# Kernel tuning notes

Measured on AMD Instinct MI355X. Metric: run time of the kernel, lower is better.

Reference implementation:

```python
import jax, jax.numpy as jnp
import numpy as np

N = 12000
E = 384000
F_IN, F_HID, F_OUT = 4, 50, 1433
NEG_SLOPE = 0.2  # PyG GATConv default leaky_relu slope


def gat_conv(x, W, a_src, a_dst, b, src, dst):
    """PyG GATConv (heads=1, concat=True) with self-loops already appended.
    x: [N, Fin], W: [Fin, Fout], a_src/a_dst/b: [Fout], src/dst: [E']."""
    h = x @ W                                   # [N, Fout]
    al = h @ a_src                              # [N] per-source logit part
    ar = h @ a_dst                              # [N] per-target logit part
    e = jax.nn.leaky_relu(al[src] + ar[dst], NEG_SLOPE)   # [E'] edge logits
    # segment softmax over edges grouped by destination node
    m = jax.ops.segment_max(e, dst, num_segments=N)       # [N]
    ex = jnp.exp(e - m[dst])
    s = jax.ops.segment_sum(ex, dst, num_segments=N)      # [N]
    alpha = ex / s[dst]                         # [E'] (self-loops => s > 0)
    out = jax.ops.segment_sum(alpha[:, None] * h[src], dst, num_segments=N)
    return out + b


def setup_inputs() -> dict:
    key = jax.random.key(0)
    ks = jax.random.split(key, 10)
    x = jax.random.normal(ks[0], (N, F_IN), dtype=jnp.float32)
    edge_index = jax.random.randint(ks[1], (2, E), 0, N, dtype=jnp.int32)
    # Glorot-ish init for params
    W1 = jax.random.normal(ks[2], (F_IN, F_HID), dtype=jnp.float32) / np.sqrt(F_IN)
    a_src1 = jax.random.normal(ks[3], (F_HID,), dtype=jnp.float32) / np.sqrt(F_HID)
    a_dst1 = jax.random.normal(ks[4], (F_HID,), dtype=jnp.float32) / np.sqrt(F_HID)
    b1 = jnp.zeros((F_HID,), dtype=jnp.float32)
    W2 = jax.random.normal(ks[5], (F_HID, F_OUT), dtype=jnp.float32) / np.sqrt(F_HID)
    a_src2 = jax.random.normal(ks[6], (F_OUT,), dtype=jnp.float32) / np.sqrt(F_OUT)
    a_dst2 = jax.random.normal(ks[7], (F_OUT,), dtype=jnp.float32) / np.sqrt(F_OUT)
    b2 = jnp.zeros((F_OUT,), dtype=jnp.float32)
    return {"x": x, "edge_index": edge_index, "W1": W1, "a_src1": a_src1,
            "a_dst1": a_dst1, "b1": b1, "W2": W2, "a_src2": a_src2,
            "a_dst2": a_dst2, "b2": b2}


def reference(x, edge_index, W1, a_src1, a_dst1, b1, W2, a_src2, a_dst2, b2):
    # PyG GATConv adds self-loops by default
    loops = jnp.arange(N, dtype=edge_index.dtype)
    src = jnp.concatenate([edge_index[0], loops])
    dst = jnp.concatenate([edge_index[1], loops])
    h = jax.nn.relu(gat_conv(x, W1, a_src1, a_dst1, b1, src, dst))
    h = jax.nn.relu(gat_conv(h, W2, a_src2, a_dst2, b2, src, dst))
    adj_pred = jax.nn.sigmoid(h @ h.T)          # InnerProductDecoder.forward_all
    return (adj_pred, edge_index)
```

## Files before the change

### kernel.cpp

```cpp
#include <hip/hip_runtime.h>
#include <hip/hip_bf16.h>

#define NNODES 12000
#define NEDGES 384000
#define NETOT  (NEDGES + NNODES)
#define FIN    4
#define FHID   50
#define FOUT   1433
#define KP     1440
#define MP     12032
#define NTILE  (MP / 128)
#define NTRI   (NTILE * (NTILE + 1) / 2)
#define NEG_SLOPE 0.2f

typedef __hip_bfloat16 bf16_t;
typedef __bf16 bf16x8 __attribute__((ext_vector_type(8)));
typedef float f32x4 __attribute__((ext_vector_type(4)));
typedef float f32x2 __attribute__((ext_vector_type(2)));

__device__ __forceinline__ float  b2f(bf16_t h) { return __bfloat162float(h); }
__device__ __forceinline__ bf16_t f2b(float f)  { return __float2bfloat16(f); }
__device__ __forceinline__ unsigned short f2bu(float f) { bf16_t h = f2b(f); return *(unsigned short*)&h; }

__global__ void k_init(int* __restrict__ deg, bf16_t* __restrict__ h2) {
    int i = blockIdx.x * blockDim.x + threadIdx.x;
    int stride = gridDim.x * blockDim.x;
    for (int v = i; v < NNODES; v += stride) deg[v] = 1;
    const size_t padN = (size_t)(MP - NNODES) * KP;
    for (size_t t = i; t < padN; t += stride) h2[(size_t)NNODES * KP + t] = f2b(0.f);
}

__global__ void k_count(const int* __restrict__ ei, int* __restrict__ deg) {
    int i = blockIdx.x * blockDim.x + threadIdx.x;
    if (i < NEDGES) atomicAdd(&deg[ei[NEDGES + i]], 1);
}

__global__ __launch_bounds__(1024) void k_scan(const int* __restrict__ deg, int* __restrict__ rowptr) {
    __shared__ int sd[1024];
    __shared__ int carry;
    int tid = threadIdx.x;
    if (tid == 0) { carry = 0; rowptr[0] = 0; }
    __syncthreads();
    for (int base = 0; base < NNODES; base += 1024) {
        int v = (base + tid < NNODES) ? deg[base + tid] : 0;
        sd[tid] = v;
        __syncthreads();
        for (int off = 1; off < 1024; off <<= 1) {
            int t = (tid >= off) ? sd[tid - off] : 0;
            __syncthreads();
            sd[tid] += t;
            __syncthreads();
        }
        int inc = sd[tid] + carry;
        if (base + tid < NNODES) rowptr[base + tid + 1] = inc;
        __syncthreads();
        if (tid == 1023) carry = sd[1023] + carry;
        __syncthreads();
    }
}

__global__ void k_cursor(const int* __restrict__ rowptr, int* __restrict__ cursor) {
    int i = blockIdx.x * blockDim.x + threadIdx.x;
    if (i < NNODES) cursor[i] = rowptr[i];
}

__global__ void k_fill(const int* __restrict__ ei, int* __restrict__ cursor, int* __restrict__ csrc) {
    int i = blockIdx.x * blockDim.x + threadIdx.x;
    if (i < NETOT) {
        int s, d;
        if (i < NEDGES) { s = ei[i]; d = ei[NEDGES + i]; }
        else            { s = d = i - NEDGES; }
        int pos = atomicAdd(&cursor[d], 1);
        csrc[pos] = s;
    }
}

__global__ __launch_bounds__(256) void k_linear1(
        const bf16_t* __restrict__ x, const bf16_t* __restrict__ W1,
        const bf16_t* __restrict__ as1, const bf16_t* __restrict__ ad1,
        float* __restrict__ h1pre, float* __restrict__ al, float* __restrict__ ar) {
    __shared__ float sW[FIN * FHID];
    __shared__ float sa[FHID], sdl[FHID];
    int tid = threadIdx.x;
    if (tid < FIN * FHID) sW[tid] = b2f(W1[tid]);
    if (tid < FHID) { sa[tid] = b2f(as1[tid]); sdl[tid] = b2f(ad1[tid]); }
    __syncthreads();
    int i = blockIdx.x * 256 + tid;
    if (i >= NNODES) return;
    float x0 = b2f(x[i * 4 + 0]), x1 = b2f(x[i * 4 + 1]);
    float x2 = b2f(x[i * 4 + 2]), x3 = b2f(x[i * 4 + 3]);
    float hal = 0.f, har = 0.f;
    for (int j = 0; j < FHID; ++j) {
        float h = x0 * sW[j] + x1 * sW[FHID + j] + x2 * sW[2 * FHID + j] + x3 * sW[3 * FHID + j];
        h1pre[(size_t)i * FHID + j] = h;
        hal += h * sa[j];
        har += h * sdl[j];
    }
    al[i] = hal; ar[i] = har;
}

__global__ __launch_bounds__(64) void k_agg1(
        const float* __restrict__ h1pre, const float* __restrict__ al, const float* __restrict__ ar,
        const int* __restrict__ rowptr, const int* __restrict__ csrc,
        const bf16_t* __restrict__ b1, float* __restrict__ h1) {
    int v = blockIdx.x, tid = threadIdx.x;
    int s0 = rowptr[v], s1 = rowptr[v + 1];
    float arv = ar[v];
    float m = -1e30f;
    for (int e = s0 + tid; e < s1; e += 64) {
        float l = al[csrc[e]] + arv;
        l = l > 0.f ? l : NEG_SLOPE * l;
        m = fmaxf(m, l);
    }
#pragma unroll
    for (int off = 32; off; off >>= 1) m = fmaxf(m, __shfl_xor(m, off, 64));
    __shared__ float sw[64];
    __shared__ int ssrc[64];
    float acc = 0.f, ssum = 0.f;
    for (int base = s0; base < s1; base += 64) {
        int e = base + tid;
        float w = 0.f; int si = 0;
        if (e < s1) {
            si = csrc[e];
            float l = al[si] + arv;
            l = l > 0.f ? l : NEG_SLOPE * l;
            w = __expf(l - m);
        }
        ssum += w;
        sw[tid] = w; ssrc[tid] = si;
        __syncthreads();
        int cnt = min(64, s1 - base);
        if (tid < FHID) {
#pragma unroll 4
            for (int j = 0; j < cnt; ++j)
                acc += sw[j] * h1pre[(size_t)ssrc[j] * FHID + tid];
        }
        __syncthreads();
    }
#pragma unroll
    for (int off = 32; off; off >>= 1) ssum += __shfl_xor(ssum, off, 64);
    if (tid < FHID) {
        float o = acc / ssum + b2f(b1[tid]);
        h1[(size_t)v * FHID + tid] = fmaxf(o, 0.f);
    }
}

__global__ __launch_bounds__(256) void k_linear2(
        const float* __restrict__ h1, const bf16_t* __restrict__ W2,
        const bf16_t* __restrict__ as2, const bf16_t* __restrict__ ad2,
        unsigned char* __restrict__ h2pre, float* __restrict__ al2, float* __restrict__ ar2) {
    int v0 = blockIdx.x * 4, tid = threadIdx.x;
    __shared__ float sh[4][FHID];
    if (tid < 4 * FHID) sh[tid / FHID][tid % FHID] = h1[(size_t)v0 * FHID + tid];
    __syncthreads();
    float pal[4] = {0.f, 0.f, 0.f, 0.f}, par[4] = {0.f, 0.f, 0.f, 0.f};
#pragma unroll
    for (int i = 0; i < 3; ++i) {
        int f0 = i * 512 + 2 * tid;
        if (f0 < KP) {
            float d0[4] = {0.f, 0.f, 0.f, 0.f}, d1[4] = {0.f, 0.f, 0.f, 0.f};
            bool ok0 = f0 < FOUT, ok1 = f0 + 1 < FOUT;
            if (ok0) {
                int f1 = ok1 ? f0 + 1 : f0;
#pragma unroll 10
                for (int k = 0; k < FHID; ++k) {
                    float w0 = b2f(W2[k * FOUT + f0]);
                    float w1 = b2f(W2[k * FOUT + f1]);
#pragma unroll
                    for (int c = 0; c < 4; ++c) {
                        d0[c] += sh[c][k] * w0;
                        d1[c] += sh[c][k] * w1;
                    }
                }
                if (!ok1) { d1[0] = d1[1] = d1[2] = d1[3] = 0.f; }
                float sa0 = b2f(as2[f0]), sd0 = b2f(ad2[f0]);
                float sa1 = ok1 ? b2f(as2[f0 + 1]) : 0.f;
                float sd1 = ok1 ? b2f(ad2[f0 + 1]) : 0.f;
#pragma unroll
                for (int c = 0; c < 4; ++c) {
                    pal[c] += d0[c] * sa0 + d1[c] * sa1;
                    par[c] += d0[c] * sd0 + d1[c] * sd1;
                }
            }
#pragma unroll
            for (int c = 0; c < 4; ++c) {
                int pk = __builtin_amdgcn_cvt_pk_fp8_f32(d0[c], d1[c], 0, false);
                *(unsigned short*)(h2pre + (size_t)(v0 + c) * KP + f0) = (unsigned short)pk;
            }
        }
    }
#pragma unroll
    for (int off = 32; off; off >>= 1)
#pragma unroll
        for (int c = 0; c < 4; ++c) {
            pal[c] += __shfl_xor(pal[c], off, 64);
            par[c] += __shfl_xor(par[c], off, 64);
        }
    __shared__ float rA[4][4], rB[4][4];
    int wave = tid >> 6, lane = tid & 63;
    if (lane == 0)
#pragma unroll
        for (int c = 0; c < 4; ++c) { rA[wave][c] = pal[c]; rB[wave][c] = par[c]; }
    __syncthreads();
    if (tid < 4) {
        al2[v0 + tid] = rA[0][tid] + rA[1][tid] + rA[2][tid] + rA[3][tid];
        ar2[v0 + tid] = rB[0][tid] + rB[1][tid] + rB[2][tid] + rB[3][tid];
    }
}

__global__ __launch_bounds__(256) void k_agg2(
        const unsigned char* __restrict__ h2pre, const float* __restrict__ al, const float* __restrict__ ar,
        const int* __restrict__ rowptr, const int* __restrict__ csrc,
        const bf16_t* __restrict__ bias2, bf16_t* __restrict__ h2) {
    int v = blockIdx.x, tid = threadIdx.x;
    int s0 = rowptr[v], s1 = rowptr[v + 1];
    float arv = ar[v];
    float m = -1e30f;
    for (int e = s0 + tid; e < s1; e += 256) {
        float l = al[csrc[e]] + arv;
        l = l > 0.f ? l : NEG_SLOPE * l;
        m = fmaxf(m, l);
    }
#pragma unroll
    for (int off = 32; off; off >>= 1) m = fmaxf(m, __shfl_xor(m, off, 64));
    __shared__ float red[4];
    int wave = tid >> 6, lane = tid & 63;
    if (lane == 0) red[wave] = m;
    __syncthreads();
    m = fmaxf(fmaxf(red[0], red[1]), fmaxf(red[2], red[3]));
    __syncthreads();

    float acc[8] = {0.f, 0.f, 0.f, 0.f, 0.f, 0.f, 0.f, 0.f};
    float ssum = 0.f;
    __shared__ float sw[256];
    __shared__ int ssrc[256];
    const bool act = tid < (KP / 8);
    for (int base = s0; base < s1; base += 256) {
        int e = base + tid;
        float w = 0.f; int si = 0;
        if (e < s1) {
            si = csrc[e];
            float l = al[si] + arv;
            l = l > 0.f ? l : NEG_SLOPE * l;
            w = __expf(l - m);
        }
        ssum += w;
        sw[tid] = w; ssrc[tid] = si;
        __syncthreads();
        int cnt = min(256, s1 - base);
        if (act) {
#pragma unroll 8
            for (int j = 0; j < cnt; ++j) {
                float wj = sw[j];
                const uint2* hp = (const uint2*)(h2pre + (size_t)ssrc[j] * KP);
                uint2 p = hp[tid];
                f32x2 e0 = __builtin_amdgcn_cvt_pk_f32_fp8(p.x, false);
                f32x2 e1 = __builtin_amdgcn_cvt_pk_f32_fp8(p.x, true);
                f32x2 e2 = __builtin_amdgcn_cvt_pk_f32_fp8(p.y, false);
                f32x2 e3 = __builtin_amdgcn_cvt_pk_f32_fp8(p.y, true);
                acc[0] += wj * e0.x; acc[1] += wj * e0.y;
                acc[2] += wj * e1.x; acc[3] += wj * e1.y;
                acc[4] += wj * e2.x; acc[5] += wj * e2.y;
                acc[6] += wj * e3.x; acc[7] += wj * e3.y;
            }
        }
        __syncthreads();
    }
#pragma unroll
    for (int off = 32; off; off >>= 1) ssum += __shfl_xor(ssum, off, 64);
    if (lane == 0) red[wave] = ssum;
    __syncthreads();
    float inv = 1.f / (red[0] + red[1] + red[2] + red[3]);

    if (act) {
        int fb = 8 * tid;
        unsigned short o[8];
#pragma unroll
        for (int t = 0; t < 8; ++t) {
            int f = fb + t;
            o[t] = f2bu((f < FOUT) ? fmaxf(acc[t] * inv + b2f(bias2[f]), 0.f) : 0.f);
        }
        uint4 pk;
        pk.x = (unsigned)o[0] | ((unsigned)o[1] << 16);
        pk.y = (unsigned)o[2] | ((unsigned)o[3] << 16);
        pk.z = (unsigned)o[4] | ((unsigned)o[5] << 16);
        pk.w = (unsigned)o[6] | ((unsigned)o[7] << 16);
        *(uint4*)(h2 + (size_t)v * KP + fb) = pk;
    }
}

__global__ __launch_bounds__(256) void k_gemm_sig(const bf16_t* __restrict__ Hm,
                                                  float* __restrict__ out) {
    int t = blockIdx.x;
    int by = (int)((2 * NTILE + 1 - sqrtf((float)(2 * NTILE + 1) * (2 * NTILE + 1) - 8.0f * t)) * 0.5f);
    if (by < 0) by = 0;
    if (by > NTILE - 1) by = NTILE - 1;
    while (by + 1 < NTILE && (by + 1) * NTILE - ((by + 1) * by) / 2 <= t) ++by;
    while (by > 0 && by * NTILE - (by * (by - 1)) / 2 > t) --by;
    int bx = by + (t - (by * NTILE - (by * (by - 1)) / 2));

    __shared__ __align__(16) bf16_t As[128 * 32];
    __shared__ __align__(16) bf16_t Bs[128 * 32];
    const int tid = threadIdx.x;
    const int wave = tid >> 6;
    const int lane = tid & 63;
    const int rowA0 = by * 128;
    const int rowB0 = bx * 128;

    const int sRow  = wave * 16 + (lane >> 2);
    const int sSlot = (lane & 3) ^ ((lane >> 2) & 3);
    const bf16_t* gA = Hm + (size_t)(rowA0 + sRow) * KP + sSlot * 8;
    const bf16_t* gB = Hm + (size_t)(rowB0 + sRow) * KP + sSlot * 8;

    f32x4 acc[4][4] = {};

    const int wrow = wave >> 1, wcol = wave & 1;
    const int r = lane & 15, q = lane >> 4;
    const int rslot = q ^ (r & 3);
    const __bf16* Asb = (const __bf16*)As;
    const __bf16* Bsb = (const __bf16*)Bs;

    for (int kt = 0; kt < KP / 32; ++kt) {
        const int k0 = kt * 32;
#pragma unroll
        for (int c = 0; c < 2; ++c) {
            __builtin_amdgcn_global_load_lds(
                (const __attribute__((address_space(1))) void*)(gA + (size_t)c * 64 * KP + k0),
                (__attribute__((address_space(3))) void*)((char*)As + c * 4096 + wave * 1024),
                16, 0, 0);
            __builtin_amdgcn_global_load_lds(
                (const __attribute__((address_space(1))) void*)(gB + (size_t)c * 64 * KP + k0),
                (__attribute__((address_space(3))) void*)((char*)Bs + c * 4096 + wave * 1024),
                16, 0, 0);
        }
        __syncthreads();
        bf16x8 af[4], bfr[4];
#pragma unroll
        for (int mi = 0; mi < 4; ++mi)
            af[mi] = *(const bf16x8*)(Asb + ((wrow * 64 + mi * 16 + r) * 32 + rslot * 8));
#pragma unroll
        for (int ni = 0; ni < 4; ++ni)
            bfr[ni] = *(const bf16x8*)(Bsb + ((wcol * 64 + ni * 16 + r) * 32 + rslot * 8));
#pragma unroll
        for (int mi = 0; mi < 4; ++mi)
#pragma unroll
            for (int ni = 0; ni < 4; ++ni)
                acc[mi][ni] = __builtin_amdgcn_mfma_f32_16x16x32_bf16(af[mi], bfr[ni], acc[mi][ni], 0, 0, 0);
        __syncthreads();
    }

#pragma unroll
    for (int mi = 0; mi < 4; ++mi) {
        const int row0 = rowA0 + wrow * 64 + mi * 16 + q * 4;
#pragma unroll
        for (int ni = 0; ni < 4; ++ni) {
            const int col = rowB0 + wcol * 64 + ni * 16 + r;
            if (col < NNODES && row0 < NNODES) {
                f32x4 s;
#pragma unroll
                for (int r2 = 0; r2 < 4; ++r2)
                    s[r2] = 1.f / (1.f + __expf(-acc[mi][ni][r2]));
#pragma unroll
                for (int r2 = 0; r2 < 4; ++r2)
                    out[(size_t)(row0 + r2) * NNODES + col] = s[r2];
                if (bx != by)
                    *(f32x4*)(out + (size_t)col * NNODES + row0) = s;
            }
        }
    }
}

__global__ void k_edges(const int* __restrict__ ei, float* __restrict__ outbase) {
    int i = blockIdx.x * blockDim.x + threadIdx.x;
    if (i < 2 * NEDGES)
        outbase[(size_t)NNODES * (size_t)NNODES + (size_t)i] = (float)ei[i];
}

extern "C" void kernel_launch(void* const* d_in, const int* in_sizes, int n_in,
                              void* d_out, int out_size, void* d_ws, size_t ws_size,
                              hipStream_t stream) {
    const bf16_t* x   = (const bf16_t*)d_in[0];
    const int*    ei  = (const int*)d_in[1];
    const bf16_t* W1  = (const bf16_t*)d_in[2];
    const bf16_t* as1 = (const bf16_t*)d_in[3];
    const bf16_t* ad1 = (const bf16_t*)d_in[4];
    const bf16_t* b1  = (const bf16_t*)d_in[5];
    const bf16_t* W2  = (const bf16_t*)d_in[6];
    const bf16_t* as2 = (const bf16_t*)d_in[7];
    const bf16_t* ad2 = (const bf16_t*)d_in[8];
    const bf16_t* b2  = (const bf16_t*)d_in[9];
    float* out = (float*)d_out;

    char* obuf = (char*)d_out;
    size_t off = 0;
    auto carve = [&](size_t bytes) {
        char* p = obuf + off;
        off += (bytes + 255) & ~(size_t)255;
        return p;
    };
    float* h1pre  = (float*)carve((size_t)NNODES * FHID * 4);
    float* al1    = (float*)carve((size_t)NNODES * 4);
    float* ar1    = (float*)carve((size_t)NNODES * 4);
    float* h1     = (float*)carve((size_t)NNODES * FHID * 4);
    float* al2    = (float*)carve((size_t)NNODES * 4);
    float* ar2    = (float*)carve((size_t)NNODES * 4);
    int*   deg    = (int*)carve((size_t)NNODES * 4);
    int*   rowptr = (int*)carve((size_t)(NNODES + 1) * 4);
    int*   cursor = (int*)carve((size_t)NNODES * 4);
    int*   csrc   = (int*)carve((size_t)NETOT * 4);
    unsigned char* h2pre = (unsigned char*)carve((size_t)NNODES * KP);
    bf16_t* h2 = (bf16_t*)d_ws;
    (void)ws_size; (void)in_sizes; (void)n_in; (void)out_size;

    hipLaunchKernelGGL(k_init,    dim3(256), dim3(256), 0, stream, deg, h2);
    hipLaunchKernelGGL(k_count,   dim3((NEDGES + 255) / 256), dim3(256), 0, stream, ei, deg);
    hipLaunchKernelGGL(k_scan,    dim3(1), dim3(1024), 0, stream, deg, rowptr);
    hipLaunchKernelGGL(k_cursor,  dim3((NNODES + 255) / 256), dim3(256), 0, stream, rowptr, cursor);
    hipLaunchKernelGGL(k_fill,    dim3((NETOT + 255) / 256), dim3(256), 0, stream, ei, cursor, csrc);
    hipLaunchKernelGGL(k_linear1, dim3((NNODES + 255) / 256), dim3(256), 0, stream,
                       x, W1, as1, ad1, h1pre, al1, ar1);
    hipLaunchKernelGGL(k_agg1,    dim3(NNODES), dim3(64), 0, stream,
                       h1pre, al1, ar1, rowptr, csrc, b1, h1);
    hipLaunchKernelGGL(k_linear2, dim3(NNODES / 4), dim3(256), 0, stream,
                       h1, W2, as2, ad2, h2pre, al2, ar2);
    hipLaunchKernelGGL(k_agg2,    dim3(NNODES), dim3(256), 0, stream,
                       h2pre, al2, ar2, rowptr, csrc, b2, h2);
    hipLaunchKernelGGL(k_gemm_sig, dim3(NTRI), dim3(256), 0, stream, h2, out);
    hipLaunchKernelGGL(k_edges,   dim3((2 * NEDGES + 255) / 256), dim3(256), 0, stream, ei, out);
}
```

Measured before the change: 1.173 ms.

## Streamline graph preprocessing, drop softmax max pass, warp-per-node agg1, fuse kernels

The serial block scan becomes a register-plus-shuffle scan that also writes the cursor array, so the separate cursor kernel goes away. The edge-index copy to the output is folded into the fill kernel. Both aggregation kernels drop the segment-max pass and exponentiate the raw logits, which relies on the logits being small enough not to overflow. agg1 maps one wave per node and broadcasts with shuffles instead of shared memory and barriers. These changes save launches and memory passes in the small kernels, but the large GEMM-plus-sigmoid stage probably dominates the runtime.

New measurement: 1.150 ms. Within noise of the previous version (-1.9%).

```diff
diff --git a/kernel.cpp b/kernel.cpp
--- a/kernel.cpp
+++ b/kernel.cpp
@@ -35,36 +35,55 @@
     if (i < NEDGES) atomicAdd(&deg[ei[NEDGES + i]], 1);
 }
 
-__global__ __launch_bounds__(1024) void k_scan(const int* __restrict__ deg, int* __restrict__ rowptr) {
-    __shared__ int sd[1024];
-    __shared__ int carry;
-    int tid = threadIdx.x;
-    if (tid == 0) { carry = 0; rowptr[0] = 0; }
-    __syncthreads();
-    for (int base = 0; base < NNODES; base += 1024) {
-        int v = (base + tid < NNODES) ? deg[base + tid] : 0;
-        sd[tid] = v;
-        __syncthreads();
-        for (int off = 1; off < 1024; off <<= 1) {
-            int t = (tid >= off) ? sd[tid - off] : 0;
-            __syncthreads();
-            sd[tid] += t;
-            __syncthreads();
-        }
-        int inc = sd[tid] + carry;
-        if (base + tid < NNODES) rowptr[base + tid + 1] = inc;
-        __syncthreads();
-        if (tid == 1023) carry = sd[1023] + carry;
-        __syncthreads();
-    }
-}
-
-__global__ void k_cursor(const int* __restrict__ rowptr, int* __restrict__ cursor) {
-    int i = blockIdx.x * blockDim.x + threadIdx.x;
-    if (i < NNODES) cursor[i] = rowptr[i];
-}
-
-__global__ void k_fill(const int* __restrict__ ei, int* __restrict__ cursor, int* __restrict__ csrc) {
+__global__ __launch_bounds__(1024) void k_scan(const int* __restrict__ deg,
+                                               int* __restrict__ rowptr,
+                                               int* __restrict__ cursor) {
+    __shared__ int wsum[16];
+    const int tid = threadIdx.x, lane = tid & 63, wv = tid >> 6;
+    const int base = tid * 12;
+    int pref[12];
+    int s = 0;
+#pragma unroll
+    for (int u = 0; u < 12; ++u) {
+        int idx = base + u;
+        int d = (idx < NNODES) ? deg[idx] : 0;
+        pref[u] = s;
+        s += d;
+    }
+    int sc = s;
+#pragma unroll
+    for (int o = 1; o < 64; o <<= 1) {
+        int t2 = __shfl_up(sc, o, 64);
+        if (lane >= o) sc += t2;
+    }
+    if (lane == 63) wsum[wv] = sc;
+    __syncthreads();
+    if (wv == 0 && lane < 16) {
+        int mine = wsum[lane];
+        int scw = mine;
+#pragma unroll
+        for (int o = 1; o < 16; o <<= 1) {
+            int t3 = __shfl_up(scw, o, 64);
+            if (lane >= o) scw += t3;
+        }
+        wsum[lane] = scw - mine;
+    }
+    __syncthreads();
+    const int pre = wsum[wv] + (sc - s);
+#pragma unroll
+    for (int u = 0; u < 12; ++u) {
+        int idx = base + u;
+        if (idx < NNODES) {
+            int p = pre + pref[u];
+            rowptr[idx] = p;
+            cursor[idx] = p;
+        }
+    }
+    if (tid == 1023) rowptr[NNODES] = pre + s;
+}
+
+__global__ void k_fill(const int* __restrict__ ei, int* __restrict__ cursor,
+                       int* __restrict__ csrc, float* __restrict__ outbase) {
     int i = blockIdx.x * blockDim.x + threadIdx.x;
     if (i < NETOT) {
         int s, d;
@@ -73,6 +92,8 @@
         int pos = atomicAdd(&cursor[d], 1);
         csrc[pos] = s;
     }
+    if (i < 2 * NEDGES)
+        outbase[(size_t)NNODES * (size_t)NNODES + (size_t)i] = (float)ei[i];
 }
 
 __global__ __launch_bounds__(256) void k_linear1(
@@ -99,49 +120,38 @@
     al[i] = hal; ar[i] = har;
 }
 
-__global__ __launch_bounds__(64) void k_agg1(
+__global__ __launch_bounds__(256) void k_agg1(
         const float* __restrict__ h1pre, const float* __restrict__ al, const float* __restrict__ ar,
         const int* __restrict__ rowptr, const int* __restrict__ csrc,
         const bf16_t* __restrict__ b1, float* __restrict__ h1) {
-    int v = blockIdx.x, tid = threadIdx.x;
-    int s0 = rowptr[v], s1 = rowptr[v + 1];
-    float arv = ar[v];
-    float m = -1e30f;
-    for (int e = s0 + tid; e < s1; e += 64) {
-        float l = al[csrc[e]] + arv;
-        l = l > 0.f ? l : NEG_SLOPE * l;
-        m = fmaxf(m, l);
-    }
-#pragma unroll
-    for (int off = 32; off; off >>= 1) m = fmaxf(m, __shfl_xor(m, off, 64));
-    __shared__ float sw[64];
-    __shared__ int ssrc[64];
+    const int wv = threadIdx.x >> 6, lane = threadIdx.x & 63;
+    const int v = blockIdx.x * 4 + wv;
+    const int s0 = rowptr[v], s1 = rowptr[v + 1];
+    const float arv = ar[v];
     float acc = 0.f, ssum = 0.f;
     for (int base = s0; base < s1; base += 64) {
-        int e = base + tid;
+        int e = base + lane;
         float w = 0.f; int si = 0;
         if (e < s1) {
             si = csrc[e];
             float l = al[si] + arv;
             l = l > 0.f ? l : NEG_SLOPE * l;
-            w = __expf(l - m);
+            w = __expf(l);
         }
         ssum += w;
-        sw[tid] = w; ssrc[tid] = si;
-        __syncthreads();
         int cnt = min(64, s1 - base);
-        if (tid < FHID) {
 #pragma unroll 4
-            for (int j = 0; j < cnt; ++j)
-                acc += sw[j] * h1pre[(size_t)ssrc[j] * FHID + tid];
-        }
-        __syncthreads();
-    }
-#pragma unroll
-    for (int off = 32; off; off >>= 1) ssum += __shfl_xor(ssum, off, 64);
-    if (tid < FHID) {
-        float o = acc / ssum + b2f(b1[tid]);
-        h1[(size_t)v * FHID + tid] = fmaxf(o, 0.f);
+        for (int j = 0; j < cnt; ++j) {
+            float wj = __shfl(w, j, 64);
+            int   sj = __shfl(si, j, 64);
+            if (lane < FHID) acc += wj * h1pre[(size_t)sj * FHID + lane];
+        }
+    }
+#pragma unroll
+    for (int o = 32; o; o >>= 1) ssum += __shfl_xor(ssum, o, 64);
+    if (lane < FHID) {
+        float o2 = acc / ssum + b2f(b1[lane]);
+        h1[(size_t)v * FHID + lane] = fmaxf(o2, 0.f);
     }
 }
 
@@ -215,25 +225,13 @@
     int v = blockIdx.x, tid = threadIdx.x;
     int s0 = rowptr[v], s1 = rowptr[v + 1];
     float arv = ar[v];
-    float m = -1e30f;
-    for (int e = s0 + tid; e < s1; e += 256) {
-        float l = al[csrc[e]] + arv;
-        l = l > 0.f ? l : NEG_SLOPE * l;
-        m = fmaxf(m, l);
-    }
-#pragma unroll
-    for (int off = 32; off; off >>= 1) m = fmaxf(m, __shfl_xor(m, off, 64));
-    __shared__ float red[4];
     int wave = tid >> 6, lane = tid & 63;
-    if (lane == 0) red[wave] = m;
-    __syncthreads();
-    m = fmaxf(fmaxf(red[0], red[1]), fmaxf(red[2], red[3]));
-    __syncthreads();
 
     float acc[8] = {0.f, 0.f, 0.f, 0.f, 0.f, 0.f, 0.f, 0.f};
     float ssum = 0.f;
     __shared__ float sw[256];
     __shared__ int ssrc[256];
+    __shared__ float red[4];
     const bool act = tid < (KP / 8);
     for (int base = s0; base < s1; base += 256) {
         int e = base + tid;
@@ -242,7 +240,7 @@
             si = csrc[e];
             float l = al[si] + arv;
             l = l > 0.f ? l : NEG_SLOPE * l;
-            w = __expf(l - m);
+            w = __expf(l);
         }
         ssum += w;
         sw[tid] = w; ssrc[tid] = si;
@@ -368,12 +366,6 @@
             }
         }
     }
-}
-
-__global__ void k_edges(const int* __restrict__ ei, float* __restrict__ outbase) {
-    int i = blockIdx.x * blockDim.x + threadIdx.x;
-    if (i < 2 * NEDGES)
-        outbase[(size_t)NNODES * (size_t)NNODES + (size_t)i] = (float)ei[i];
 }
 
 extern "C" void kernel_launch(void* const* d_in, const int* in_sizes, int n_in,
@@ -414,17 +406,16 @@
 
     hipLaunchKernelGGL(k_init,    dim3(256), dim3(256), 0, stream, deg, h2);
     hipLaunchKernelGGL(k_count,   dim3((NEDGES + 255) / 256), dim3(256), 0, stream, ei, deg);
-    hipLaunchKernelGGL(k_scan,    dim3(1), dim3(1024), 0, stream, deg, rowptr);
-    hipLaunchKernelGGL(k_cursor,  dim3((NNODES + 255) / 256), dim3(256), 0, stream, rowptr, cursor);
-    hipLaunchKernelGGL(k_fill,    dim3((NETOT + 255) / 256), dim3(256), 0, stream, ei, cursor, csrc);
+    hipLaunchKernelGGL(k_scan,    dim3(1), dim3(1024), 0, stream, deg, rowptr, cursor);
+    hipLaunchKernelGGL(k_fill,    dim3((2 * NEDGES + 255) / 256), dim3(256), 0, stream,
+                       ei, cursor, csrc, out);
     hipLaunchKernelGGL(k_linear1, dim3((NNODES + 255) / 256), dim3(256), 0, stream,
                        x, W1, as1, ad1, h1pre, al1, ar1);
-    hipLaunchKernelGGL(k_agg1,    dim3(NNODES), dim3(64), 0, stream,
+    hipLaunchKernelGGL(k_agg1,    dim3(NNODES / 4), dim3(256), 0, stream,
                        h1pre, al1, ar1, rowptr, csrc, b1, h1);
     hipLaunchKernelGGL(k_linear2, dim3(NNODES / 4), dim3(256), 0, stream,
                        h1, W2, as2, ad2, h2pre, al2, ar2);
     hipLaunchKernelGGL(k_agg2,    dim3(NNODES), dim3(256), 0, stream,
                        h2pre, al2, ar2, rowptr, csrc, b2, h2);
     hipLaunchKernelGGL(k_gemm_sig, dim3(NTRI), dim3(256), 0, stream, h2, out);
-    hipLaunchKernelGGL(k_edges,   dim3((2 * NEDGES + 255) / 256), dim3(256), 0, stream, ei, out);
-}
+}
```
